# Performance work log

Hardware: AMD Instinct MI355X
Metric: run time of the kernel (lower is better)

Reference implementation:

```python
import jax, jax.numpy as jnp
import numpy as np

TEMPLATERES = 192
RENDER = 180
XDIM = RENDER // 2  # 90
TOPK = 4


def make_gridF():
    half = TEMPLATERES // 2
    x_idx = jnp.arange(XDIM + 1, dtype=jnp.float32) / float(half)
    y_idx = jnp.arange(-XDIM, XDIM + 1, dtype=jnp.float32) / float(half)
    yg, xg = jnp.meshgrid(y_idx, x_idx, indexing='ij')  # [181,91]
    zg = jnp.zeros_like(xg)
    return jnp.stack([xg, yg, zg], axis=-1)[None, None]  # [1,1,181,91,3]


def grid_sample_3d(vol, grid):
    # vol: [B,C,D,H,W]; grid: [B,Do,Ho,Wo,3] with xyz in [-1,1].
    # Trilinear, align_corners=True, zero padding (matches F.grid_sample defaults).
    B, C, D, H, W = vol.shape
    x = (grid[..., 0] + 1.0) * 0.5 * (W - 1)
    y = (grid[..., 1] + 1.0) * 0.5 * (H - 1)
    z = (grid[..., 2] + 1.0) * 0.5 * (D - 1)
    x0 = jnp.floor(x); y0 = jnp.floor(y); z0 = jnp.floor(z)
    wx = x - x0; wy = y - y0; wz = z - z0

    def gather(zi, yi, xi):
        valid = ((zi >= 0) & (zi < D) & (yi >= 0) & (yi < H) & (xi >= 0) & (xi < W)).astype(vol.dtype)
        zc = jnp.clip(zi, 0, D - 1).astype(jnp.int32)
        yc = jnp.clip(yi, 0, H - 1).astype(jnp.int32)
        xc = jnp.clip(xi, 0, W - 1).astype(jnp.int32)
        v = jax.vmap(lambda vb, zb, yb, xb: vb[:, zb, yb, xb])(vol, zc, yc, xc)  # [B,C,Do,Ho,Wo]
        return v * valid[:, None]

    out = jnp.zeros((B, C) + grid.shape[1:4], dtype=vol.dtype)
    for zi, wzc in ((z0, 1.0 - wz), (z0 + 1, wz)):
        for yi, wyc in ((y0, 1.0 - wy), (y0 + 1, wy)):
            for xi, wxc in ((x0, 1.0 - wx), (x0 + 1, wx)):
                out = out + gather(zi, yi, xi) * (wzc * wyc * wxc)[:, None]
    return out


def setup_inputs() -> dict:
    key = jax.random.key(0)
    k1, k2, k3 = jax.random.split(key, 3)
    src = jax.random.normal(k1, (8, 2, TEMPLATERES, TEMPLATERES, TEMPLATERES), jnp.float32)
    rot = jax.random.normal(k2, (8, 1, 1, 3, 3), jnp.float32)
    ref_fft = jax.random.normal(k3, (8, 1, RENDER, XDIM + 1, 2), jnp.float32)
    return {"src": src, "rot": rot, "ref_fft": ref_fft, "gridF": make_gridF()}


def reference(src, rot, ref_fft, gridF):
    # --- rotate_and_sampleFT: sample central slice of the Fourier volume ---
    pos = jnp.matmul(gridF, rot)                       # [B,1,181,91,3]
    sampled = grid_sample_3d(src, pos)                 # [B,2,1,181,91]
    s = jnp.moveaxis(sampled, 1, -1)                   # [B,1,181,91,2]
    scale = float(RENDER ** 2) / float(TEMPLATERES ** 3)
    sc = (s[..., 0] + 1j * s[..., 1]) * scale          # complex [B,1,181,91]
    sH = sc[..., :RENDER, :]                           # [B,1,180,91]
    sH = jnp.fft.fftshift(sH, axes=-2)
    # --- local_transl_search: FFT cross-correlation + top-k translations ---
    ref = ref_fft[..., 0] + 1j * ref_fft[..., 1]       # [B,1,180,91]
    cross = sH * jnp.conj(ref)
    r = jnp.fft.irfft2(cross, axes=(-2, -1))           # [B,1,180,180]
    B = r.shape[0]
    width = r.shape[-1]
    vals, inds = jax.lax.top_k(r.reshape(B, -1), TOPK)  # sorted=True, matches torch.topk(sorted=True)
    r_k_val = 2.0 * vals                               # [B,4]
    trans = jnp.stack([inds % width, inds // width], axis=-1) - width // 2
    return r_k_val, trans.astype(jnp.float32)
```

## Files before the change

kernel.cpp:

```cpp
#include <hip/hip_runtime.h>

#define NB 8
#define NY 180
#define NKX 91
#define NV 192
#define SCALEF (75.0f/16384.0f)

typedef unsigned long long ull;

__device__ __forceinline__ unsigned int enc_f(float v) {
    unsigned int u = __float_as_uint(v);
    return (u & 0x80000000u) ? ~u : (u | 0x80000000u);
}
__device__ __forceinline__ float dec_f(unsigned int u) {
    return __uint_as_float((u & 0x80000000u) ? (u & 0x7FFFFFFFu) : ~u);
}

__global__ __launch_bounds__(192) void k_sample_colfft(
    const float* __restrict__ src, const float* __restrict__ rot,
    const float* __restrict__ ref, float* __restrict__ T)
{
    const int blk = blockIdx.x;
    const int b = blk / NKX, kx = blk - b * NKX;
    const int t = threadIdx.x;

    __shared__ float Gr[NY], Gi[NY];
    __shared__ float ctab[NY], stab[NY];

    if (t < NY) {
        double a = (double)t * (6.283185307179586476925286766559 / 180.0);
        ctab[t] = (float)cos(a);
        stab[t] = (float)sin(a);
    }

    if (t < NY) {
        int i = t + 90; if (i >= NY) i -= NY;
        float xg = (float)kx / 96.0f;
        float yg = (float)(i - 90) / 96.0f;
        const float* R = rot + (size_t)b * 9;
        float p0 = xg * R[0] + yg * R[3];
        float p1 = xg * R[1] + yg * R[4];
        float p2 = xg * R[2] + yg * R[5];
        float fx = (p0 + 1.0f) * 0.5f * 191.0f;
        float fy = (p1 + 1.0f) * 0.5f * 191.0f;
        float fz = (p2 + 1.0f) * 0.5f * 191.0f;
        float x0 = floorf(fx), y0 = floorf(fy), z0 = floorf(fz);
        float wx = fx - x0, wy = fy - y0, wz = fz - z0;

        float s0 = 0.f, s1 = 0.f;
        const float* vb = src + (size_t)b * 2u * NV * NV * NV;
        #pragma unroll
        for (int dz = 0; dz < 2; ++dz) {
            float zi = z0 + (float)dz;
            float wzc = dz ? wz : 1.0f - wz;
            bool vz = (zi >= 0.f) && (zi < (float)NV);
            int zc = (int)fminf(fmaxf(zi, 0.f), (float)(NV - 1));
            #pragma unroll
            for (int dy = 0; dy < 2; ++dy) {
                float yi = y0 + (float)dy;
                float wyc = dy ? wy : 1.0f - wy;
                bool vy = (yi >= 0.f) && (yi < (float)NV);
                int yc = (int)fminf(fmaxf(yi, 0.f), (float)(NV - 1));
                #pragma unroll
                for (int dx = 0; dx < 2; ++dx) {
                    float xi = x0 + (float)dx;
                    float wxc = dx ? wx : 1.0f - wx;
                    bool vx = (xi >= 0.f) && (xi < (float)NV);
                    int xc = (int)fminf(fmaxf(xi, 0.f), (float)(NV - 1));
                    if (vz && vy && vx) {
                        float w = wzc * wyc * wxc;
                        size_t off = ((size_t)zc * NV + (size_t)yc) * NV + (size_t)xc;
                        s0 += vb[off] * w;
                        s1 += vb[(size_t)NV * NV * NV + off] * w;
                    }
                }
            }
        }
        s0 *= SCALEF; s1 *= SCALEF;

        const float* rp = ref + (((size_t)b * NY + (size_t)t) * NKX + (size_t)kx) * 2u;
        float rr = rp[0], ri = rp[1];
        float cr = s0 * rr + s1 * ri;
        float ci = s1 * rr - s0 * ri;
        float f = (kx == 0 || kx == NKX - 1) ? (2.0f / 32400.0f) : (4.0f / 32400.0f);
        Gr[t] = cr * f;
        Gi[t] = ci * f;
    }
    __syncthreads();

    if (t < NY) {
        float ar = 0.f, ai = 0.f;
        int idx = 0;
        for (int ky = 0; ky < NY; ++ky) {
            float c = ctab[idx], s = stab[idx];
            float gr = Gr[ky], gi = Gi[ky];
            ar += gr * c - gi * s;
            ai += gr * s + gi * c;
            idx += t; if (idx >= NY) idx -= NY;
        }
        float* Tp = T + (((size_t)b * NY + (size_t)t) * NKX + (size_t)kx) * 2u;
        Tp[0] = ar; Tp[1] = ai;
    }
}

__global__ __launch_bounds__(256) void k_rowfft_topk(
    const float* __restrict__ T, ull* __restrict__ cand)
{
    const int blk = blockIdx.x;
    const int b = blk / NY, y = blk - b * NY;
    const int t = threadIdx.x;

    __shared__ float Trow[2 * NKX];
    __shared__ float ctab[NY], stab[NY];
    __shared__ ull sm[256];

    if (t < NY) {
        double a = (double)t * (6.283185307179586476925286766559 / 180.0);
        ctab[t] = (float)cos(a);
        stab[t] = (float)sin(a);
    }
    {
        const float* Tp = T + ((size_t)(b * NY + y) * NKX) * 2u;
        if (t < 2 * NKX) Trow[t] = Tp[t];
    }
    __syncthreads();

    ull my = 0;
    if (t < NY) {
        float acc = 0.f;
        int idx = 0;
        for (int kx = 0; kx < NKX; ++kx) {
            acc += Trow[2 * kx] * ctab[idx] - Trow[2 * kx + 1] * stab[idx];
            idx += t; if (idx >= NY) idx -= NY;
        }
        int flat = y * NY + t;
        my = ((ull)enc_f(acc) << 32) | (ull)(0x7FFFFFFFu - (unsigned int)flat);
    }

    for (int r = 0; r < 4; ++r) {
        sm[t] = my;
        __syncthreads();
        #pragma unroll
        for (int s = 128; s > 0; s >>= 1) {
            if (t < s) { ull o = sm[t + s]; if (o > sm[t]) sm[t] = o; }
            __syncthreads();
        }
        ull win = sm[0];
        if (t == 0) cand[(size_t)blk * 4 + r] = win;
        __syncthreads();
        if (my == win) my = 0;
    }
}

__global__ __launch_bounds__(256) void k_final(
    const ull* __restrict__ cand, float* __restrict__ out)
{
    const int b = blockIdx.x;
    const int t = threadIdx.x;
    __shared__ ull sm[256];

    ull loc[3];
    #pragma unroll
    for (int k = 0; k < 3; ++k) {
        int i = t + k * 256;
        loc[k] = (i < NY * 4) ? cand[(size_t)b * NY * 4 + i] : 0;
    }

    for (int r = 0; r < 4; ++r) {
        ull m = loc[0];
        if (loc[1] > m) m = loc[1];
        if (loc[2] > m) m = loc[2];
        sm[t] = m;
        __syncthreads();
        #pragma unroll
        for (int s = 128; s > 0; s >>= 1) {
            if (t < s) { ull o = sm[t + s]; if (o > sm[t]) sm[t] = o; }
            __syncthreads();
        }
        ull win = sm[0];
        __syncthreads();
        #pragma unroll
        for (int k = 0; k < 3; ++k) if (loc[k] == win) loc[k] = 0;
        if (t == 0) {
            float val = dec_f((unsigned int)(win >> 32));
            int flat = (int)(0x7FFFFFFFu - (unsigned int)(win & 0xFFFFFFFFu));
            int x = flat % NY, yy = flat / NY;
            out[b * 4 + r] = val;
            out[32 + (b * 4 + r) * 2 + 0] = (float)(x - NY / 2);
            out[32 + (b * 4 + r) * 2 + 1] = (float)(yy - NY / 2);
        }
    }
}

extern "C" void kernel_launch(void* const* d_in, const int* in_sizes, int n_in,
                              void* d_out, int out_size, void* d_ws, size_t ws_size,
                              hipStream_t stream) {
    const float* src = (const float*)d_in[0];
    const float* rot = (const float*)d_in[1];
    const float* ref = (const float*)d_in[2];
    float* out = (float*)d_out;

    float* T = (float*)d_ws;
    ull* cand = (ull*)((char*)d_ws + (size_t)NB * NY * NKX * 2 * 4);

    k_sample_colfft<<<dim3(NB * NKX), dim3(192), 0, stream>>>(src, rot, ref, T);
    k_rowfft_topk<<<dim3(NB * NY), dim3(256), 0, stream>>>(T, cand);
    k_final<<<dim3(NB), dim3(256), 0, stream>>>(cand, out);
}
```

Measured before the change: 530.1 us.

## Batch trilinear gathers, use twiddle recurrence, and wave-shuffle top-k reductions

Restructures the trilinear sampling so all 8 offsets and weights are computed first and the 16 gathers are issued together, giving more memory-level parallelism. Replaces shared-memory cos/sin tables in both DFT stages with a per-thread complex rotation recurrence seeded by one double-precision sincos. Replaces the 256-wide shared-memory tree max reductions with 64-lane shuffle reductions plus a small cross-wave step, cutting barriers. The recurrence can accumulate rounding error over 180 steps, which could perturb near-tied top-k ordering.

```diff
diff --git a/kernel.cpp b/kernel.cpp
--- a/kernel.cpp
+++ b/kernel.cpp
@@ -5,6 +5,7 @@
 #define NKX 91
 #define NV 192
 #define SCALEF (75.0f/16384.0f)
+#define TWOPI_180 0.034906585039886591538473815369772
 
 typedef unsigned long long ull;
 
@@ -15,6 +16,7 @@
 __device__ __forceinline__ float dec_f(unsigned int u) {
     return __uint_as_float((u & 0x80000000u) ? (u & 0x7FFFFFFFu) : ~u);
 }
+__device__ __forceinline__ ull umax64(ull a, ull b) { return a > b ? a : b; }
 
 __global__ __launch_bounds__(192) void k_sample_colfft(
     const float* __restrict__ src, const float* __restrict__ rot,
@@ -25,13 +27,6 @@
     const int t = threadIdx.x;
 
     __shared__ float Gr[NY], Gi[NY];
-    __shared__ float ctab[NY], stab[NY];
-
-    if (t < NY) {
-        double a = (double)t * (6.283185307179586476925286766559 / 180.0);
-        ctab[t] = (float)cos(a);
-        stab[t] = (float)sin(a);
-    }
 
     if (t < NY) {
         int i = t + 90; if (i >= NY) i -= NY;
@@ -47,35 +42,32 @@
         float x0 = floorf(fx), y0 = floorf(fy), z0 = floorf(fz);
         float wx = fx - x0, wy = fy - y0, wz = fz - z0;
 
+        const float* vb = src + (size_t)b * 2u * NV * NV * NV;
+        const size_t choff = (size_t)NV * NV * NV;
+        float wgt[8];
+        size_t off[8];
+        bool vld[8];
+        #pragma unroll
+        for (int k = 0; k < 8; ++k) {
+            int dz = k >> 2, dy = (k >> 1) & 1, dx = k & 1;
+            float zi = z0 + (float)dz, yi = y0 + (float)dy, xi = x0 + (float)dx;
+            vld[k] = (zi >= 0.f) && (zi < (float)NV) && (yi >= 0.f) && (yi < (float)NV)
+                  && (xi >= 0.f) && (xi < (float)NV);
+            int zc = (int)fminf(fmaxf(zi, 0.f), (float)(NV - 1));
+            int yc = (int)fminf(fmaxf(yi, 0.f), (float)(NV - 1));
+            int xc = (int)fminf(fmaxf(xi, 0.f), (float)(NV - 1));
+            off[k] = ((size_t)zc * NV + (size_t)yc) * NV + (size_t)xc;
+            wgt[k] = (dz ? wz : 1.0f - wz) * (dy ? wy : 1.0f - wy) * (dx ? wx : 1.0f - wx);
+        }
+        float v0[8], v1[8];
+        #pragma unroll
+        for (int k = 0; k < 8; ++k) {
+            v0[k] = vld[k] ? vb[off[k]] : 0.0f;
+            v1[k] = vld[k] ? vb[choff + off[k]] : 0.0f;
+        }
         float s0 = 0.f, s1 = 0.f;
-        const float* vb = src + (size_t)b * 2u * NV * NV * NV;
-        #pragma unroll
-        for (int dz = 0; dz < 2; ++dz) {
-            float zi = z0 + (float)dz;
-            float wzc = dz ? wz : 1.0f - wz;
-            bool vz = (zi >= 0.f) && (zi < (float)NV);
-            int zc = (int)fminf(fmaxf(zi, 0.f), (float)(NV - 1));
-            #pragma unroll
-            for (int dy = 0; dy < 2; ++dy) {
-                float yi = y0 + (float)dy;
-                float wyc = dy ? wy : 1.0f - wy;
-                bool vy = (yi >= 0.f) && (yi < (float)NV);
-                int yc = (int)fminf(fmaxf(yi, 0.f), (float)(NV - 1));
-                #pragma unroll
-                for (int dx = 0; dx < 2; ++dx) {
-                    float xi = x0 + (float)dx;
-                    float wxc = dx ? wx : 1.0f - wx;
-                    bool vx = (xi >= 0.f) && (xi < (float)NV);
-                    int xc = (int)fminf(fmaxf(xi, 0.f), (float)(NV - 1));
-                    if (vz && vy && vx) {
-                        float w = wzc * wyc * wxc;
-                        size_t off = ((size_t)zc * NV + (size_t)yc) * NV + (size_t)xc;
-                        s0 += vb[off] * w;
-                        s1 += vb[(size_t)NV * NV * NV + off] * w;
-                    }
-                }
-            }
-        }
+        #pragma unroll
+        for (int k = 0; k < 8; ++k) { s0 += v0[k] * wgt[k]; s1 += v1[k] * wgt[k]; }
         s0 *= SCALEF; s1 *= SCALEF;
 
         const float* rp = ref + (((size_t)b * NY + (size_t)t) * NKX + (size_t)kx) * 2u;
@@ -89,14 +81,17 @@
     __syncthreads();
 
     if (t < NY) {
+        double a = (double)t * TWOPI_180;
+        float c1 = (float)cos(a), s1 = (float)sin(a);
+        float c = 1.0f, s = 0.0f;
         float ar = 0.f, ai = 0.f;
-        int idx = 0;
         for (int ky = 0; ky < NY; ++ky) {
-            float c = ctab[idx], s = stab[idx];
             float gr = Gr[ky], gi = Gi[ky];
             ar += gr * c - gi * s;
             ai += gr * s + gi * c;
-            idx += t; if (idx >= NY) idx -= NY;
+            float cn = c * c1 - s * s1;
+            s = c * s1 + s * c1;
+            c = cn;
         }
         float* Tp = T + (((size_t)b * NY + (size_t)t) * NKX + (size_t)kx) * 2u;
         Tp[0] = ar; Tp[1] = ai;
@@ -109,16 +104,11 @@
     const int blk = blockIdx.x;
     const int b = blk / NY, y = blk - b * NY;
     const int t = threadIdx.x;
+    const int lane = t & 63, wid = t >> 6;
 
     __shared__ float Trow[2 * NKX];
-    __shared__ float ctab[NY], stab[NY];
-    __shared__ ull sm[256];
-
-    if (t < NY) {
-        double a = (double)t * (6.283185307179586476925286766559 / 180.0);
-        ctab[t] = (float)cos(a);
-        stab[t] = (float)sin(a);
-    }
+    __shared__ ull sm[8];
+
     {
         const float* Tp = T + ((size_t)(b * NY + y) * NKX) * 2u;
         if (t < 2 * NKX) Trow[t] = Tp[t];
@@ -127,27 +117,36 @@
 
     ull my = 0;
     if (t < NY) {
+        double a = (double)t * TWOPI_180;
+        float c1 = (float)cos(a), s1 = (float)sin(a);
+        float c = 1.0f, s = 0.0f;
         float acc = 0.f;
-        int idx = 0;
         for (int kx = 0; kx < NKX; ++kx) {
-            acc += Trow[2 * kx] * ctab[idx] - Trow[2 * kx + 1] * stab[idx];
-            idx += t; if (idx >= NY) idx -= NY;
+            acc += Trow[2 * kx] * c - Trow[2 * kx + 1] * s;
+            float cn = c * c1 - s * s1;
+            s = c * s1 + s * c1;
+            c = cn;
         }
         int flat = y * NY + t;
         my = ((ull)enc_f(acc) << 32) | (ull)(0x7FFFFFFFu - (unsigned int)flat);
     }
 
     for (int r = 0; r < 4; ++r) {
-        sm[t] = my;
-        __syncthreads();
-        #pragma unroll
-        for (int s = 128; s > 0; s >>= 1) {
-            if (t < s) { ull o = sm[t + s]; if (o > sm[t]) sm[t] = o; }
-            __syncthreads();
-        }
-        ull win = sm[0];
+        ull m = my;
+        #pragma unroll
+        for (int k = 32; k >= 1; k >>= 1)
+            m = umax64(m, (ull)__shfl_xor((long long)m, k));
+        if (lane == 0) sm[wid] = m;
+        __syncthreads();
+        if (t == 0) {
+            ull w = sm[0];
+            #pragma unroll
+            for (int i = 1; i < 4; ++i) w = umax64(w, sm[i]);
+            sm[4] = w;
+        }
+        __syncthreads();
+        ull win = sm[4];
         if (t == 0) cand[(size_t)blk * 4 + r] = win;
-        __syncthreads();
         if (my == win) my = 0;
     }
 }
@@ -157,7 +156,8 @@
 {
     const int b = blockIdx.x;
     const int t = threadIdx.x;
-    __shared__ ull sm[256];
+    const int lane = t & 63, wid = t >> 6;
+    __shared__ ull sm[8];
 
     ull loc[3];
     #pragma unroll
@@ -167,18 +167,20 @@
     }
 
     for (int r = 0; r < 4; ++r) {
-        ull m = loc[0];
-        if (loc[1] > m) m = loc[1];
-        if (loc[2] > m) m = loc[2];
-        sm[t] = m;
-        __syncthreads();
-        #pragma unroll
-        for (int s = 128; s > 0; s >>= 1) {
-            if (t < s) { ull o = sm[t + s]; if (o > sm[t]) sm[t] = o; }
-            __syncthreads();
-        }
-        ull win = sm[0];
-        __syncthreads();
+        ull m = umax64(umax64(loc[0], loc[1]), loc[2]);
+        #pragma unroll
+        for (int k = 32; k >= 1; k >>= 1)
+            m = umax64(m, (ull)__shfl_xor((long long)m, k));
+        if (lane == 0) sm[wid] = m;
+        __syncthreads();
+        if (t == 0) {
+            ull w = sm[0];
+            #pragma unroll
+            for (int i = 1; i < 4; ++i) w = umax64(w, sm[i]);
+            sm[4] = w;
+        }
+        __syncthreads();
+        ull win = sm[4];
         #pragma unroll
         for (int k = 0; k < 3; ++k) if (loc[k] == win) loc[k] = 0;
         if (t == 0) {
@@ -189,6 +191,7 @@
             out[32 + (b * 4 + r) * 2 + 0] = (float)(x - NY / 2);
             out[32 + (b * 4 + r) * 2 + 1] = (float)(yy - NY / 2);
         }
+        __syncthreads();
     }
 }
 
```

After: 521.9 us. About the same (-1.5%).
